# Kernel tuning notes

Hardware: AMD Instinct MI355X
Metric: run time of the kernel (lower is better)

The kernel has to match this reference:

```python
import jax, jax.numpy as jnp
import numpy as np

I_DIM, K_DIM, V_DIM, O_DIM = 64, 64, 32, 64
P, NH, NK = 7, 2, 4
B, H, W = 8, 256, 256


def get_unfold_params_v2(width, kernel_size, num_kernels):
    # exact replica of the torch helper's search
    if width <= kernel_size:
        return width, 1, 1, 1
    if width <= kernel_size + num_kernels:
        return kernel_size, 1, 1, width - kernel_size + 1

    def _sd(nk):
        d = 1
        while True:
            k = (kernel_size - 1) * d + 1
            if (width - k) % (nk - 1) == 0:
                return (width - k) // (nk - 1), d
            d += 1
            if d >= kernel_size:
                return None, d

    while True:
        s, d = _sd(num_kernels)
        if s and s < (kernel_size - 1) * d + 1:
            return kernel_size, s, d, num_kernels
        num_kernels += 1


def conv1x1(x, Wt, b):
    # x: [B,C,H,W], Wt: [O,C]
    return jnp.einsum('oc,bchw->bohw', Wt, x) + b[None, :, None, None]


def to_patches(x, nh, idx, p):
    # x: [B,C,H,W] -> [B, nh, nph*npw, C//nh, p*p] (unfold + rearrange)
    Bs, C, _, _ = x.shape
    hd = C // nh
    npw = idx.shape[0]
    pt = x[:, :, idx][:, :, :, :, idx]          # [B,C,nph,ph,npw,pw]
    pt = pt.reshape(Bs, nh, hd, npw, p, npw, p)
    pt = pt.transpose(0, 1, 3, 5, 2, 4, 6)       # B,nh,nph,npw,hd,ph,pw
    return pt.reshape(Bs, nh, npw * npw, hd, p * p)


def from_patches(o, nh, idx, p, Hh, Ww):
    # o: [B,nh,S,hd,p*p] -> fold (overlap scatter-add) -> [B, nh*hd, H, W]
    Bs, _, _, hd, _ = o.shape
    npw = idx.shape[0]
    o = o.reshape(Bs, nh, npw, npw, hd, p, p)
    o = o.transpose(0, 1, 4, 2, 5, 3, 6)         # B,nh,hd,nph,ph,npw,pw
    o = o.reshape(Bs, nh * hd, npw, p, npw, p)
    out = jnp.zeros((Bs, nh * hd, Hh, Ww), o.dtype)
    return out.at[:, :, idx[:, :, None, None], idx[None, None, :, :]].add(o)


def setup_inputs() -> dict:
    key = jax.random.key(0)
    ks = jax.random.split(key, 8)
    s = 0.05
    return {
        'x1': jax.random.normal(ks[0], (B, I_DIM, H, W), jnp.float32),
        'x2': jax.random.normal(ks[1], (B, I_DIM, H, W), jnp.float32),
        'Wk': jax.random.normal(ks[2], (2 * K_DIM, I_DIM), jnp.float32) * s,
        'bk': jax.random.normal(ks[3], (2 * K_DIM,), jnp.float32) * s,
        'Wv': jax.random.normal(ks[4], (2 * V_DIM, I_DIM), jnp.float32) * s,
        'bv': jax.random.normal(ks[5], (2 * V_DIM,), jnp.float32) * s,
        'Wp': jax.random.normal(ks[6], (O_DIM, 2 * V_DIM), jnp.float32) * s,
        'bp': jax.random.normal(ks[7], (O_DIM,), jnp.float32) * s,
    }


def reference(x1, x2, Wk, bk, Wv, bv, Wp, bp):
    _, _, Hh, Ww = x1.shape
    p, stride, dilation, nkrn = get_unfold_params_v2(Ww, P, NK)
    idx = np.arange(nkrn)[:, None] * stride + np.arange(p)[None, :] * dilation  # [npw,p]

    # grouped 1x1 convs (groups=2): split weights into per-stream halves
    k1 = conv1x1(x1, Wk[:K_DIM], bk[:K_DIM])
    k2 = conv1x1(x2, Wk[K_DIM:], bk[K_DIM:])
    v1 = conv1x1(x1, Wv[:V_DIM], bv[:V_DIM])
    v2 = conv1x1(x2, Wv[V_DIM:], bv[V_DIM:])

    k1p = to_patches(k1, NH, idx, p)  # [B,nh,S,hd_k,pp]
    k2p = to_patches(k2, NH, idx, p)
    v1p = to_patches(v1, NH, idx, p)  # [B,nh,S,hd_v,pp]
    v2p = to_patches(v2, NH, idx, p)

    scale = k1p.shape[-2] ** (-0.5)
    kk = jnp.einsum('bnsdx,bnsdy->bnsxy', k1p * scale, k2p)  # [B,nh,S,pp,pp]
    a1 = jax.nn.softmax(kk, axis=-2)
    o1 = jnp.einsum('bnsxy,bnsdx->bnsdy', a1, v1p)
    a2 = jax.nn.softmax(kk, axis=-1)
    o2 = jnp.einsum('bnsxy,bnsdy->bnsdx', a2, v2p)

    o1 = from_patches(o1, NH, idx, p, Hh, Ww)  # [B,V_DIM,H,W]
    o2 = from_patches(o2, NH, idx, p, Hh, Ww)
    o = jnp.concatenate([o1, o2], axis=1)      # [B,2*V_DIM,H,W]
    return conv1x1(o, Wp, bp)                  # [B,O_DIM,H,W]
```

## Files before the change

kernel.cpp:

```cpp
#include <hip/hip_runtime.h>

#define BB 8
#define HH 256
#define CIN 64
#define NPW 12
#define SPP 144
#define PP 49
#define PDIM 7
#define STRIDE 21
#define DIL 4
#define NS 84
#define HDK 32
#define HDV 16

static __device__ __forceinline__ unsigned short f2bf(float f) {
  union { float f; unsigned u; } v; v.f = f;
  unsigned r = (v.u + 0x7fffu + ((v.u >> 16) & 1u)) >> 16;
  return (unsigned short)r;
}
static __device__ __forceinline__ float bf2f(unsigned short h) {
  union { unsigned u; float f; } v; v.u = ((unsigned)h) << 16;
  return v.f;
}

__global__ __launch_bounds__(256, 3) void k1_fused(
    const float* __restrict__ x1, const float* __restrict__ x2,
    const float* __restrict__ Wk, const float* __restrict__ bk,
    const float* __restrict__ Wv, const float* __restrict__ bv,
    const float* __restrict__ Wp, float* __restrict__ P)
{
  __shared__ unsigned short kv[192][52];
  __shared__ union UU {
    float xs[2][CIN][50];
    struct {
      float A1[49][50];
      float A2[49][50];
      float rmax[49], rsum[49], cmax[49], csum[49];
      float O[64][50];
    } a;
  } u;

  const int tid = threadIdx.x;
  const int blk = blockIdx.x;
  const int b  = blk / SPP;
  const int s  = blk % SPP;
  const int pi = s / NPW, pj = s % NPW;
  const int h0 = pi * STRIDE, w0 = pj * STRIDE;

  for (int i = tid; i < 2 * CIN * PP; i += 256) {
    int src = i / (CIN * PP);
    int r = i - src * (CIN * PP);
    int c = r / PP, t = r - c * PP;
    int ph = t / PDIM, pw = t - ph * PDIM;
    const float* xp = src ? x2 : x1;
    u.xs[src][c][t] =
        xp[(((size_t)b * CIN + c) * HH + (h0 + ph * DIL)) * HH + (w0 + pw * DIL)];
  }
  __syncthreads();

  for (int task = tid; task < 48 * 13; task += 256) {
    int g = task / 13, tg = task % 13;
    int row0 = g * 4, t0 = tg * 4;
    int tc[4];
    #pragma unroll
    for (int j = 0; j < 4; j++) tc[j] = min(t0 + j, PP - 1);
    int src = (row0 < 64) ? 0 : (row0 < 128 ? 1 : (row0 < 160 ? 0 : 1));
    const float* wbase;
    float bias[4];
    if (row0 < 128) {
      wbase = Wk + row0 * 64;
      #pragma unroll
      for (int i = 0; i < 4; i++) bias[i] = bk[row0 + i];
    } else {
      wbase = Wv + (row0 - 128) * 64;
      #pragma unroll
      for (int i = 0; i < 4; i++) bias[i] = bv[row0 - 128 + i];
    }
    const float* xsrc = &u.xs[src][0][0];
    float acc[4][4];
    #pragma unroll
    for (int i = 0; i < 4; i++)
      #pragma unroll
      for (int j = 0; j < 4; j++) acc[i][j] = 0.f;
    for (int c = 0; c < 64; c++) {
      float wv0 = wbase[c], wv1 = wbase[64 + c], wv2 = wbase[128 + c], wv3 = wbase[192 + c];
      #pragma unroll
      for (int j = 0; j < 4; j++) {
        float xv = xsrc[c * 50 + tc[j]];
        acc[0][j] += wv0 * xv; acc[1][j] += wv1 * xv;
        acc[2][j] += wv2 * xv; acc[3][j] += wv3 * xv;
      }
    }
    #pragma unroll
    for (int i = 0; i < 4; i++)
      #pragma unroll
      for (int j = 0; j < 4; j++)
        if (t0 + j < PP) kv[row0 + i][t0 + j] = f2bf(acc[i][j] + bias[i]);
  }
  __syncthreads();

  const float scale = 0.17677669529663687f;

  for (int n = 0; n < 2; n++) {
    for (int task = tid; task < 13 * 13; task += 256) {
      int xg = task / 13, yg = task % 13;
      int x0 = xg * 4, y0 = yg * 4;
      int xc[4], yc[4];
      #pragma unroll
      for (int j = 0; j < 4; j++) { xc[j] = min(x0 + j, 48); yc[j] = min(y0 + j, 48); }
      float acc[4][4];
      #pragma unroll
      for (int i = 0; i < 4; i++)
        #pragma unroll
        for (int j = 0; j < 4; j++) acc[i][j] = 0.f;
      for (int d = 0; d < HDK; d++) {
        const unsigned short* k1r = kv[n * HDK + d];
        const unsigned short* k2r = kv[64 + n * HDK + d];
        float a0 = bf2f(k1r[xc[0]]), a1v = bf2f(k1r[xc[1]]);
        float a2v = bf2f(k1r[xc[2]]), a3v = bf2f(k1r[xc[3]]);
        float b0 = bf2f(k2r[yc[0]]), b1v = bf2f(k2r[yc[1]]);
        float b2v = bf2f(k2r[yc[2]]), b3v = bf2f(k2r[yc[3]]);
        acc[0][0] += a0 * b0;  acc[0][1] += a0 * b1v;  acc[0][2] += a0 * b2v;  acc[0][3] += a0 * b3v;
        acc[1][0] += a1v * b0; acc[1][1] += a1v * b1v; acc[1][2] += a1v * b2v; acc[1][3] += a1v * b3v;
        acc[2][0] += a2v * b0; acc[2][1] += a2v * b1v; acc[2][2] += a2v * b2v; acc[2][3] += a2v * b3v;
        acc[3][0] += a3v * b0; acc[3][1] += a3v * b1v; acc[3][2] += a3v * b2v; acc[3][3] += a3v * b3v;
      }
      #pragma unroll
      for (int i = 0; i < 4; i++)
        if (x0 + i < 49)
          #pragma unroll
          for (int j = 0; j < 4; j++)
            if (y0 + j < 49) u.a.A1[x0 + i][y0 + j] = acc[i][j] * scale;
    }
    __syncthreads();

    if (tid < 98) {
      int isRow = tid >= 49;
      int j = tid - (isRow ? 49 : 0);
      float m = -1e30f;
      for (int k = 0; k < 49; k++) {
        float v = isRow ? u.a.A1[j][k] : u.a.A1[k][j];
        m = fmaxf(m, v);
      }
      float sm = 0.f;
      for (int k = 0; k < 49; k++) {
        float v = isRow ? u.a.A1[j][k] : u.a.A1[k][j];
        sm += __expf(v - m);
      }
      if (isRow) { u.a.rmax[j] = m; u.a.rsum[j] = 1.0f / sm; }
      else       { u.a.cmax[j] = m; u.a.csum[j] = 1.0f / sm; }
    }
    __syncthreads();

    for (int i = tid; i < 49 * 49; i += 256) {
      int x = i / 49, y = i - x * 49;
      float v = u.a.A1[x][y];
      u.a.A2[x][y] = __expf(v - u.a.rmax[x]) * u.a.rsum[x];
      u.a.A1[x][y] = __expf(v - u.a.cmax[y]) * u.a.csum[y];
    }
    __syncthreads();

    for (int task = tid; task < 2 * 4 * 13; task += 256) {
      int which = task / 52;
      int r = task - which * 52;
      int dg = r / 13, tg = r % 13;
      int d0 = dg * 4, t0 = tg * 4;
      int tc[4];
      #pragma unroll
      for (int j = 0; j < 4; j++) tc[j] = min(t0 + j, 48);
      float acc[4][4];
      #pragma unroll
      for (int i = 0; i < 4; i++)
        #pragma unroll
        for (int j = 0; j < 4; j++) acc[i][j] = 0.f;
      if (which == 0) {
        for (int x = 0; x < 49; x++) {
          float a0 = u.a.A1[x][tc[0]], a1v = u.a.A1[x][tc[1]];
          float a2v = u.a.A1[x][tc[2]], a3v = u.a.A1[x][tc[3]];
          #pragma unroll
          for (int i = 0; i < 4; i++) {
            float vv = bf2f(kv[128 + n * HDV + d0 + i][x]);
            acc[i][0] += vv * a0; acc[i][1] += vv * a1v;
            acc[i][2] += vv * a2v; acc[i][3] += vv * a3v;
          }
        }
      } else {
        for (int y = 0; y < 49; y++) {
          float a0 = u.a.A2[tc[0]][y], a1v = u.a.A2[tc[1]][y];
          float a2v = u.a.A2[tc[2]][y], a3v = u.a.A2[tc[3]][y];
          #pragma unroll
          for (int i = 0; i < 4; i++) {
            float vv = bf2f(kv[160 + n * HDV + d0 + i][y]);
            acc[i][0] += vv * a0; acc[i][1] += vv * a1v;
            acc[i][2] += vv * a2v; acc[i][3] += vv * a3v;
          }
        }
      }
      #pragma unroll
      for (int i = 0; i < 4; i++)
        #pragma unroll
        for (int j = 0; j < 4; j++)
          if (t0 + j < 49) u.a.O[which * 32 + n * HDV + d0 + i][t0 + j] = acc[i][j];
    }
    __syncthreads();
  }

  for (int task = tid; task < 16 * 13; task += 256) {
    int ocg = task / 13, tg = task % 13;
    int oc0 = ocg * 4, t0 = tg * 4;
    int tc[4];
    #pragma unroll
    for (int j = 0; j < 4; j++) tc[j] = min(t0 + j, 48);
    float acc[4][4];
    #pragma unroll
    for (int i = 0; i < 4; i++)
      #pragma unroll
      for (int j = 0; j < 4; j++) acc[i][j] = 0.f;
    #pragma unroll 4
    for (int l = 0; l < 64; l++) {
      float w0 = Wp[(oc0 + 0) * 64 + l];
      float w1 = Wp[(oc0 + 1) * 64 + l];
      float w2 = Wp[(oc0 + 2) * 64 + l];
      float w3 = Wp[(oc0 + 3) * 64 + l];
      float o0 = u.a.O[l][tc[0]], o1v = u.a.O[l][tc[1]];
      float o2v = u.a.O[l][tc[2]], o3v = u.a.O[l][tc[3]];
      acc[0][0] += w0 * o0; acc[0][1] += w0 * o1v; acc[0][2] += w0 * o2v; acc[0][3] += w0 * o3v;
      acc[1][0] += w1 * o0; acc[1][1] += w1 * o1v; acc[1][2] += w1 * o2v; acc[1][3] += w1 * o3v;
      acc[2][0] += w2 * o0; acc[2][1] += w2 * o1v; acc[2][2] += w2 * o2v; acc[2][3] += w2 * o3v;
      acc[3][0] += w3 * o0; acc[3][1] += w3 * o1v; acc[3][2] += w3 * o2v; acc[3][3] += w3 * o3v;
    }
    #pragma unroll
    for (int i = 0; i < 4; i++) {
      #pragma unroll
      for (int j = 0; j < 4; j++) {
        int t = t0 + j;
        if (t < 49) {
          int ph = t / 7, pw = t - ph * 7;
          P[(((size_t)b * 64 + (oc0 + i)) * NS + (pi * 7 + ph)) * NS + (pj * 7 + pw)] =
              acc[i][j];
        }
      }
    }
  }
}

__global__ __launch_bounds__(256) void k2_merge(
    const float* __restrict__ P, const float* __restrict__ bp,
    float* __restrict__ out)
{
  __shared__ float bps[64];
  __shared__ int wsmap[256];
  const int tid = threadIdx.x;
  const int b = blockIdx.x / HH, h = blockIdx.x % HH;
  if (tid < 64) bps[tid] = bp[tid];
  {
    int w = tid, wsv = -1;
    for (int pj = 0; pj < NPW; pj++) {
      int r = w - pj * STRIDE;
      if (r >= 0 && r <= (PDIM - 1) * DIL && (r % DIL) == 0) { wsv = pj * PDIM + r / DIL; break; }
    }
    wsmap[tid] = wsv;
  }
  int hs = -1;
  for (int pi = 0; pi < NPW; pi++) {
    int r = h - pi * STRIDE;
    if (r >= 0 && r <= (PDIM - 1) * DIL && (r % DIL) == 0) { hs = pi * PDIM + r / DIL; break; }
  }
  __syncthreads();

  const int wq = tid & 63;
  const int ocq = tid >> 6;
  float4* out4 = (float4*)out;

  if (hs < 0) {
    #pragma unroll 4
    for (int oc = ocq; oc < 64; oc += 4) {
      float bv = bps[oc];
      out4[(((size_t)b * 64 + oc) * HH + h) * 64 + wq] = make_float4(bv, bv, bv, bv);
    }
    return;
  }
  const int ws0 = wsmap[wq * 4 + 0], ws1 = wsmap[wq * 4 + 1];
  const int ws2 = wsmap[wq * 4 + 2], ws3 = wsmap[wq * 4 + 3];
  #pragma unroll 4
  for (int oc = ocq; oc < 64; oc += 4) {
    float bv = bps[oc];
    size_t rbase = (((size_t)b * 64 + oc) * NS + hs) * NS;
    float4 v = make_float4(bv, bv, bv, bv);
    if (ws0 >= 0) v.x += P[rbase + ws0];
    if (ws1 >= 0) v.y += P[rbase + ws1];
    if (ws2 >= 0) v.z += P[rbase + ws2];
    if (ws3 >= 0) v.w += P[rbase + ws3];
    out4[(((size_t)b * 64 + oc) * HH + h) * 64 + wq] = v;
  }
}

extern "C" void kernel_launch(void* const* d_in, const int* in_sizes, int n_in,
                              void* d_out, int out_size, void* d_ws, size_t ws_size,
                              hipStream_t stream) {
  const float* x1 = (const float*)d_in[0];
  const float* x2 = (const float*)d_in[1];
  const float* Wk = (const float*)d_in[2];
  const float* bk = (const float*)d_in[3];
  const float* Wv = (const float*)d_in[4];
  const float* bv = (const float*)d_in[5];
  const float* Wp = (const float*)d_in[6];
  const float* bp = (const float*)d_in[7];
  float* P = (float*)d_ws;
  float* out = (float*)d_out;

  k1_fused<<<dim3(BB * SPP), dim3(256), 0, stream>>>(x1, x2, Wk, bk, Wv, bv, Wp, P);
  k2_merge<<<dim3(BB * HH), dim3(256), 0, stream>>>(P, bp, out);
}
```

Measured before the change: 414.3 us.

## Store LDS tiles in bf16, fuse softmax exp into PV, process both heads concurrently

Shared-memory buffers for the inputs, attention logits and outputs become bf16 instead of fp32, which shrinks the LDS footprint and lets the launch bound rise to 4 blocks per CU. The per-head loop is removed: both heads' QK, softmax statistics and PV run at once across the thread block, with fewer barriers. The normalized attention matrices are no longer materialized; exp is recomputed inside the PV loop and the normalisation is applied at the end. Loads become vectorized ushort4 reads. This adds rounding from storing logits in bf16 and repeats the exp work.

```diff
diff --git a/kernel.cpp b/kernel.cpp
--- a/kernel.cpp
+++ b/kernel.cpp
@@ -12,6 +12,7 @@
 #define NS 84
 #define HDK 32
 #define HDV 16
+#define RS 52
 
 static __device__ __forceinline__ unsigned short f2bf(float f) {
   union { float f; unsigned u; } v; v.f = f;
@@ -23,20 +24,20 @@
   return v.f;
 }
 
-__global__ __launch_bounds__(256, 3) void k1_fused(
+__global__ __launch_bounds__(256, 4) void k1_fused(
     const float* __restrict__ x1, const float* __restrict__ x2,
     const float* __restrict__ Wk, const float* __restrict__ bk,
     const float* __restrict__ Wv, const float* __restrict__ bv,
     const float* __restrict__ Wp, float* __restrict__ P)
 {
-  __shared__ unsigned short kv[192][52];
+  __shared__ unsigned short kv[192][RS];
   __shared__ union UU {
-    float xs[2][CIN][50];
+    unsigned short xs[2][CIN][RS];
     struct {
-      float A1[49][50];
-      float A2[49][50];
-      float rmax[49], rsum[49], cmax[49], csum[49];
-      float O[64][50];
+      unsigned short kkb[2][49][RS];
+      unsigned short O[64][RS];
+      float cmax[2][49], csum[2][49];
+      float rmax[2][49], rsum[2][49];
     } a;
   } u;
 
@@ -53,17 +54,14 @@
     int c = r / PP, t = r - c * PP;
     int ph = t / PDIM, pw = t - ph * PDIM;
     const float* xp = src ? x2 : x1;
-    u.xs[src][c][t] =
-        xp[(((size_t)b * CIN + c) * HH + (h0 + ph * DIL)) * HH + (w0 + pw * DIL)];
+    float v = xp[(((size_t)b * CIN + c) * HH + (h0 + ph * DIL)) * HH + (w0 + pw * DIL)];
+    u.xs[src][c][t] = f2bf(v);
   }
   __syncthreads();
 
   for (int task = tid; task < 48 * 13; task += 256) {
     int g = task / 13, tg = task % 13;
     int row0 = g * 4, t0 = tg * 4;
-    int tc[4];
-    #pragma unroll
-    for (int j = 0; j < 4; j++) tc[j] = min(t0 + j, PP - 1);
     int src = (row0 < 64) ? 0 : (row0 < 128 ? 1 : (row0 < 160 ? 0 : 1));
     const float* wbase;
     float bias[4];
@@ -76,7 +74,7 @@
       #pragma unroll
       for (int i = 0; i < 4; i++) bias[i] = bv[row0 - 128 + i];
     }
-    const float* xsrc = &u.xs[src][0][0];
+    const unsigned short* xsrc = &u.xs[src][0][0];
     float acc[4][4];
     #pragma unroll
     for (int i = 0; i < 4; i++)
@@ -84,11 +82,12 @@
       for (int j = 0; j < 4; j++) acc[i][j] = 0.f;
     for (int c = 0; c < 64; c++) {
       float wv0 = wbase[c], wv1 = wbase[64 + c], wv2 = wbase[128 + c], wv3 = wbase[192 + c];
+      ushort4 x4 = *(const ushort4*)&xsrc[c * RS + t0];
+      float xv[4] = { bf2f(x4.x), bf2f(x4.y), bf2f(x4.z), bf2f(x4.w) };
       #pragma unroll
       for (int j = 0; j < 4; j++) {
-        float xv = xsrc[c * 50 + tc[j]];
-        acc[0][j] += wv0 * xv; acc[1][j] += wv1 * xv;
-        acc[2][j] += wv2 * xv; acc[3][j] += wv3 * xv;
+        acc[0][j] += wv0 * xv[j]; acc[1][j] += wv1 * xv[j];
+        acc[2][j] += wv2 * xv[j]; acc[3][j] += wv3 * xv[j];
       }
     }
     #pragma unroll
@@ -101,116 +100,123 @@
 
   const float scale = 0.17677669529663687f;
 
-  for (int n = 0; n < 2; n++) {
-    for (int task = tid; task < 13 * 13; task += 256) {
-      int xg = task / 13, yg = task % 13;
-      int x0 = xg * 4, y0 = yg * 4;
-      int xc[4], yc[4];
-      #pragma unroll
-      for (int j = 0; j < 4; j++) { xc[j] = min(x0 + j, 48); yc[j] = min(y0 + j, 48); }
-      float acc[4][4];
+  if (tid < 182) {
+    int n = tid / 91;
+    int r = tid % 91;
+    int xg = r / 7, yg = r % 7;
+    int x0 = xg * 4, y0 = yg * 7;
+    float acc[4][7];
+    #pragma unroll
+    for (int i = 0; i < 4; i++)
+      #pragma unroll
+      for (int j = 0; j < 7; j++) acc[i][j] = 0.f;
+    for (int d = 0; d < HDK; d++) {
+      const unsigned short* k1r = kv[n * HDK + d];
+      const unsigned short* k2r = kv[64 + n * HDK + d];
+      ushort4 a4 = *(const ushort4*)&k1r[x0];
+      float av[4] = { bf2f(a4.x), bf2f(a4.y), bf2f(a4.z), bf2f(a4.w) };
+      float bvv[7];
+      #pragma unroll
+      for (int j = 0; j < 7; j++) bvv[j] = bf2f(k2r[y0 + j]);
       #pragma unroll
       for (int i = 0; i < 4; i++)
         #pragma unroll
-        for (int j = 0; j < 4; j++) acc[i][j] = 0.f;
-      for (int d = 0; d < HDK; d++) {
-        const unsigned short* k1r = kv[n * HDK + d];
-        const unsigned short* k2r = kv[64 + n * HDK + d];
-        float a0 = bf2f(k1r[xc[0]]), a1v = bf2f(k1r[xc[1]]);
-        float a2v = bf2f(k1r[xc[2]]), a3v = bf2f(k1r[xc[3]]);
-        float b0 = bf2f(k2r[yc[0]]), b1v = bf2f(k2r[yc[1]]);
-        float b2v = bf2f(k2r[yc[2]]), b3v = bf2f(k2r[yc[3]]);
-        acc[0][0] += a0 * b0;  acc[0][1] += a0 * b1v;  acc[0][2] += a0 * b2v;  acc[0][3] += a0 * b3v;
-        acc[1][0] += a1v * b0; acc[1][1] += a1v * b1v; acc[1][2] += a1v * b2v; acc[1][3] += a1v * b3v;
-        acc[2][0] += a2v * b0; acc[2][1] += a2v * b1v; acc[2][2] += a2v * b2v; acc[2][3] += a2v * b3v;
-        acc[3][0] += a3v * b0; acc[3][1] += a3v * b1v; acc[3][2] += a3v * b2v; acc[3][3] += a3v * b3v;
+        for (int j = 0; j < 7; j++) acc[i][j] += av[i] * bvv[j];
+    }
+    #pragma unroll
+    for (int i = 0; i < 4; i++)
+      if (x0 + i < 49)
+        #pragma unroll
+        for (int j = 0; j < 7; j++)
+          u.a.kkb[n][x0 + i][y0 + j] = f2bf(acc[i][j] * scale);
+  }
+  __syncthreads();
+
+  if (tid < 196) {
+    int n = tid / 98;
+    int r = tid % 98;
+    int isRow = r >= 49;
+    int j = r - (isRow ? 49 : 0);
+    float m = -1e30f;
+    for (int k = 0; k < 49; k++) {
+      float v = bf2f(isRow ? u.a.kkb[n][j][k] : u.a.kkb[n][k][j]);
+      m = fmaxf(m, v);
+    }
+    float sm = 0.f;
+    for (int k = 0; k < 49; k++) {
+      float v = bf2f(isRow ? u.a.kkb[n][j][k] : u.a.kkb[n][k][j]);
+      sm += __expf(v - m);
+    }
+    if (isRow) { u.a.rmax[n][j] = m; u.a.rsum[n][j] = 1.0f / sm; }
+    else       { u.a.cmax[n][j] = m; u.a.csum[n][j] = 1.0f / sm; }
+  }
+  __syncthreads();
+
+  if (tid < 208) {
+    int n = tid / 104;
+    int r = tid % 104;
+    int side = r / 52;
+    int r2 = r % 52;
+    int dg = r2 / 13, tg = r2 % 13;
+    int d0 = dg * 4, t0 = tg * 4;
+    int tc[4];
+    #pragma unroll
+    for (int j = 0; j < 4; j++) tc[j] = min(t0 + j, 48);
+    float acc[4][4];
+    #pragma unroll
+    for (int i = 0; i < 4; i++)
+      #pragma unroll
+      for (int j = 0; j < 4; j++) acc[i][j] = 0.f;
+    if (side == 0) {
+      float cm[4];
+      #pragma unroll
+      for (int j = 0; j < 4; j++) cm[j] = u.a.cmax[n][tc[j]];
+      for (int x = 0; x < 49; x++) {
+        ushort4 k4 = *(const ushort4*)&u.a.kkb[n][x][t0];
+        float e[4] = { __expf(bf2f(k4.x) - cm[0]), __expf(bf2f(k4.y) - cm[1]),
+                       __expf(bf2f(k4.z) - cm[2]), __expf(bf2f(k4.w) - cm[3]) };
+        #pragma unroll
+        for (int i = 0; i < 4; i++) {
+          float vv = bf2f(kv[128 + n * HDV + d0 + i][x]);
+          acc[i][0] += vv * e[0]; acc[i][1] += vv * e[1];
+          acc[i][2] += vv * e[2]; acc[i][3] += vv * e[3];
+        }
       }
       #pragma unroll
       for (int i = 0; i < 4; i++)
-        if (x0 + i < 49)
-          #pragma unroll
-          for (int j = 0; j < 4; j++)
-            if (y0 + j < 49) u.a.A1[x0 + i][y0 + j] = acc[i][j] * scale;
-    }
-    __syncthreads();
-
-    if (tid < 98) {
-      int isRow = tid >= 49;
-      int j = tid - (isRow ? 49 : 0);
-      float m = -1e30f;
-      for (int k = 0; k < 49; k++) {
-        float v = isRow ? u.a.A1[j][k] : u.a.A1[k][j];
-        m = fmaxf(m, v);
-      }
-      float sm = 0.f;
-      for (int k = 0; k < 49; k++) {
-        float v = isRow ? u.a.A1[j][k] : u.a.A1[k][j];
-        sm += __expf(v - m);
-      }
-      if (isRow) { u.a.rmax[j] = m; u.a.rsum[j] = 1.0f / sm; }
-      else       { u.a.cmax[j] = m; u.a.csum[j] = 1.0f / sm; }
-    }
-    __syncthreads();
-
-    for (int i = tid; i < 49 * 49; i += 256) {
-      int x = i / 49, y = i - x * 49;
-      float v = u.a.A1[x][y];
-      u.a.A2[x][y] = __expf(v - u.a.rmax[x]) * u.a.rsum[x];
-      u.a.A1[x][y] = __expf(v - u.a.cmax[y]) * u.a.csum[y];
-    }
-    __syncthreads();
-
-    for (int task = tid; task < 2 * 4 * 13; task += 256) {
-      int which = task / 52;
-      int r = task - which * 52;
-      int dg = r / 13, tg = r % 13;
-      int d0 = dg * 4, t0 = tg * 4;
-      int tc[4];
-      #pragma unroll
-      for (int j = 0; j < 4; j++) tc[j] = min(t0 + j, 48);
-      float acc[4][4];
+        #pragma unroll
+        for (int j = 0; j < 4; j++)
+          if (t0 + j < 49)
+            u.a.O[n * HDV + d0 + i][t0 + j] = f2bf(acc[i][j] * u.a.csum[n][t0 + j]);
+    } else {
+      float rm[4];
+      #pragma unroll
+      for (int j = 0; j < 4; j++) rm[j] = u.a.rmax[n][tc[j]];
+      for (int y = 0; y < 49; y++) {
+        float e[4];
+        #pragma unroll
+        for (int j = 0; j < 4; j++)
+          e[j] = __expf(bf2f(u.a.kkb[n][tc[j]][y]) - rm[j]);
+        #pragma unroll
+        for (int i = 0; i < 4; i++) {
+          float vv = bf2f(kv[160 + n * HDV + d0 + i][y]);
+          acc[i][0] += vv * e[0]; acc[i][1] += vv * e[1];
+          acc[i][2] += vv * e[2]; acc[i][3] += vv * e[3];
+        }
+      }
       #pragma unroll
       for (int i = 0; i < 4; i++)
         #pragma unroll
-        for (int j = 0; j < 4; j++) acc[i][j] = 0.f;
-      if (which == 0) {
-        for (int x = 0; x < 49; x++) {
-          float a0 = u.a.A1[x][tc[0]], a1v = u.a.A1[x][tc[1]];
-          float a2v = u.a.A1[x][tc[2]], a3v = u.a.A1[x][tc[3]];
-          #pragma unroll
-          for (int i = 0; i < 4; i++) {
-            float vv = bf2f(kv[128 + n * HDV + d0 + i][x]);
-            acc[i][0] += vv * a0; acc[i][1] += vv * a1v;
-            acc[i][2] += vv * a2v; acc[i][3] += vv * a3v;
-          }
-        }
-      } else {
-        for (int y = 0; y < 49; y++) {
-          float a0 = u.a.A2[tc[0]][y], a1v = u.a.A2[tc[1]][y];
-          float a2v = u.a.A2[tc[2]][y], a3v = u.a.A2[tc[3]][y];
-          #pragma unroll
-          for (int i = 0; i < 4; i++) {
-            float vv = bf2f(kv[160 + n * HDV + d0 + i][y]);
-            acc[i][0] += vv * a0; acc[i][1] += vv * a1v;
-            acc[i][2] += vv * a2v; acc[i][3] += vv * a3v;
-          }
-        }
-      }
-      #pragma unroll
-      for (int i = 0; i < 4; i++)
-        #pragma unroll
         for (int j = 0; j < 4; j++)
-          if (t0 + j < 49) u.a.O[which * 32 + n * HDV + d0 + i][t0 + j] = acc[i][j];
-    }
-    __syncthreads();
-  }
-
-  for (int task = tid; task < 16 * 13; task += 256) {
-    int ocg = task / 13, tg = task % 13;
+          if (t0 + j < 49)
+            u.a.O[32 + n * HDV + d0 + i][t0 + j] = f2bf(acc[i][j] * u.a.rsum[n][t0 + j]);
+    }
+  }
+  __syncthreads();
+
+  if (tid < 208) {
+    int ocg = tid / 13, tg = tid % 13;
     int oc0 = ocg * 4, t0 = tg * 4;
-    int tc[4];
-    #pragma unroll
-    for (int j = 0; j < 4; j++) tc[j] = min(t0 + j, 48);
     float acc[4][4];
     #pragma unroll
     for (int i = 0; i < 4; i++)
@@ -222,12 +228,13 @@
       float w1 = Wp[(oc0 + 1) * 64 + l];
       float w2 = Wp[(oc0 + 2) * 64 + l];
       float w3 = Wp[(oc0 + 3) * 64 + l];
-      float o0 = u.a.O[l][tc[0]], o1v = u.a.O[l][tc[1]];
-      float o2v = u.a.O[l][tc[2]], o3v = u.a.O[l][tc[3]];
-      acc[0][0] += w0 * o0; acc[0][1] += w0 * o1v; acc[0][2] += w0 * o2v; acc[0][3] += w0 * o3v;
-      acc[1][0] += w1 * o0; acc[1][1] += w1 * o1v; acc[1][2] += w1 * o2v; acc[1][3] += w1 * o3v;
-      acc[2][0] += w2 * o0; acc[2][1] += w2 * o1v; acc[2][2] += w2 * o2v; acc[2][3] += w2 * o3v;
-      acc[3][0] += w3 * o0; acc[3][1] += w3 * o1v; acc[3][2] += w3 * o2v; acc[3][3] += w3 * o3v;
+      ushort4 o4 = *(const ushort4*)&u.a.O[l][t0];
+      float ov[4] = { bf2f(o4.x), bf2f(o4.y), bf2f(o4.z), bf2f(o4.w) };
+      #pragma unroll
+      for (int j = 0; j < 4; j++) {
+        acc[0][j] += w0 * ov[j]; acc[1][j] += w1 * ov[j];
+        acc[2][j] += w2 * ov[j]; acc[3][j] += w3 * ov[j];
+      }
     }
     #pragma unroll
     for (int i = 0; i < 4; i++) {
```

Measured after the change: 407.4 us. Within noise of the previous version (-1.7%).
